# Optimization experiments

Measured on AMD Instinct MI355X. Metric: run time of the kernel, lower is better.

Reference implementation:

```python
import jax, jax.numpy as jnp
import numpy as np

K = 3
KK = K * K
G = 8  # num_heads / offset groups
PAD = K // 2


def conv2d(x, w, b):
    # NCHW conv, stride 1, same padding
    y = jax.lax.conv_general_dilated(
        x, w, window_strides=(1, 1), padding=[(PAD, PAD), (PAD, PAD)],
        dimension_numbers=("NCHW", "OIHW", "NCHW"))
    return y + b[None, :, None, None]


def bilinear_sample(img, py, px):
    # img: [Cg, H, W]; py/px: [KK, H, W] fractional sampling locations
    # zero-padding bilinear (torchvision deform_conv2d semantics)
    Cg, H, W = img.shape
    flat = img.reshape(Cg, H * W)

    y0 = jnp.floor(py)
    x0 = jnp.floor(px)
    wy1 = py - y0
    wx1 = px - x0
    wy0 = 1.0 - wy1
    wx0 = 1.0 - wx1
    y0i = y0.astype(jnp.int32)
    x0i = x0.astype(jnp.int32)

    def gather(iy, ix):
        valid = (iy >= 0) & (iy < H) & (ix >= 0) & (ix < W)
        idx = jnp.clip(iy, 0, H - 1) * W + jnp.clip(ix, 0, W - 1)
        v = jnp.take(flat, idx.reshape(-1), axis=1).reshape(Cg, KK, H, W)
        return v * valid[None].astype(img.dtype)

    return (gather(y0i, x0i) * (wy0 * wx0)[None]
            + gather(y0i, x0i + 1) * (wy0 * wx1)[None]
            + gather(y0i + 1, x0i) * (wy1 * wx0)[None]
            + gather(y0i + 1, x0i + 1) * (wy1 * wx1)[None])


def setup_inputs() -> dict:
    key = jax.random.key(0)
    ks = jax.random.split(key, 8)
    B, C, H, W = 8, 256, 64, 64
    O = 256
    x = jax.random.normal(ks[0], (B, C, H, W), jnp.float32)
    w_off = jax.random.normal(ks[1], (2 * KK * G, C, K, K), jnp.float32) * 0.01
    b_off = jax.random.normal(ks[2], (2 * KK * G,), jnp.float32) * 0.01
    w_attn = jax.random.normal(ks[3], (KK * G, C, K, K), jnp.float32) * 0.01
    b_attn = jax.random.normal(ks[4], (KK * G,), jnp.float32) * 0.01
    w_out = jax.random.normal(ks[5], (O, C, K, K), jnp.float32) * 0.02
    b_out = jax.random.normal(ks[6], (O,), jnp.float32) * 0.01
    return {"x": x, "w_off": w_off, "b_off": b_off,
            "w_attn": w_attn, "b_attn": b_attn,
            "w_out": w_out, "b_out": b_out}


def reference(x, w_off, b_off, w_attn, b_attn, w_out, b_out):
    B, C, H, W = x.shape
    O = w_out.shape[0]
    Cg = C // G

    # learned offsets: [B, G, KK, 2(dy,dx), H, W]
    off = conv2d(x, w_off, b_off).reshape(B, G, KK, 2, H, W)
    # modulation mask with softmax over the KK kernel taps (per head)
    attn = conv2d(x, w_attn, b_attn).reshape(B, G, KK, H, W)
    attn = jax.nn.softmax(attn, axis=2)

    # base sampling grid for each kernel tap (stride=1, dilation=1)
    ki = (jnp.arange(KK) // K).astype(x.dtype)  # kernel row
    kj = (jnp.arange(KK) % K).astype(x.dtype)   # kernel col
    base_y = jnp.arange(H, dtype=x.dtype)[None, :, None] - PAD + ki[:, None, None]  # [KK,H,1]
    base_x = jnp.arange(W, dtype=x.dtype)[None, None, :] - PAD + kj[:, None, None]  # [KK,1,W]
    py = base_y + off[:, :, :, 0]  # [B,G,KK,H,W]
    px = base_x + off[:, :, :, 1]

    xg = x.reshape(B, G, Cg, H, W)
    # vmap bilinear gather over batch and offset groups -> [B,G,Cg,KK,H,W]
    samp = jax.vmap(jax.vmap(bilinear_sample))(xg, py, px)

    # modulated deformable conv: mask-weight the samples, contract with weights
    wt = w_out.reshape(O, G, Cg, KK)
    out = jnp.einsum("bgnkhw,bgkhw,ognk->bohw", samp, attn, wt)
    return out + b_out[None, :, None, None]
```

## Files before the change

kernel.cpp:

```cpp
#include <hip/hip_runtime.h>

#define BN   8
#define CC   256
#define HH   64
#define WW   64
#define GG   8
#define CG   32
#define KKK  9
#define OO   256
#define HW   (HH*WW)
#define NPAD 256
#define NOUT 216

typedef __attribute__((ext_vector_type(8))) _Float16 half8;
typedef __attribute__((ext_vector_type(4))) float f32x4;

union U4H8 { uint4 u; half8 h; };

#define LGKM0_BARRIER() do { \
    asm volatile("s_waitcnt lgkmcnt(0)" ::: "memory"); \
    __builtin_amdgcn_s_barrier(); \
    __builtin_amdgcn_sched_barrier(0); \
} while (0)

__global__ void repack_w(const float* __restrict__ w_out, _Float16* __restrict__ wt3) {
    int idx = blockIdx.x * 256 + threadIdx.x;
    if (idx >= GG * KKK * CG * OO) return;
    int e    = idx & 7;
    int lane = (idx >> 3) & 63;
    int ot   = (idx >> 9) & 15;
    int s    = idx >> 13;
    int kk = s % 9;
    int g  = s / 9;
    int oc = ot * 16 + (lane & 15);
    int cg = (lane >> 4) * 8 + e;
    wt3[idx] = (_Float16)w_out[oc * 2304 + (g * 32 + cg) * 9 + kk];
}

__global__ void repack_conv(const float* __restrict__ w_off, const float* __restrict__ b_off,
                            const float* __restrict__ w_attn, const float* __restrict__ b_attn,
                            _Float16* __restrict__ wt_conv, float* __restrict__ bias_c) {
    int idx = blockIdx.x * 256 + threadIdx.x;
    if (idx >= 9 * NPAD * 256) return;
    int e    = idx & 7;
    int lane = (idx >> 3) & 63;
    int ot   = (idx >> 9) & 15;
    int gs   = idx >> 13;
    int tap = gs >> 3;
    int ch  = (gs & 7) * 32 + (lane >> 4) * 8 + e;
    int n   = ot * 16 + (lane & 15);
    float v = 0.f;
    if (n < 144)      v = w_off[(n * 256 + ch) * 9 + tap];
    else if (n < 216) v = w_attn[((n - 144) * 256 + ch) * 9 + tap];
    wt_conv[idx] = (_Float16)v;
    if (idx < 224) {
        float bv = 0.f;
        if (idx < 144)      bv = b_off[idx];
        else if (idx < 216) bv = b_attn[idx - 144];
        bias_c[idx] = bv;
    }
}

__global__ __launch_bounds__(256) void repack_x(const float* __restrict__ x,
                                                _Float16* __restrict__ x_h) {
    __shared__ _Float16 T[64][264];
    const int bid = blockIdx.x;
    const int b = bid & 7, h = bid >> 3;
    const int t = threadIdx.x;
    const float* src = x + (((long)(b * 256 + t)) << 12) + h * 64;
    #pragma unroll
    for (int i = 0; i < 16; ++i) {
        float4 f = ((const float4*)src)[i];
        T[i * 4 + 0][t] = (_Float16)f.x;
        T[i * 4 + 1][t] = (_Float16)f.y;
        T[i * 4 + 2][t] = (_Float16)f.z;
        T[i * 4 + 3][t] = (_Float16)f.w;
    }
    __syncthreads();
    _Float16* dst = x_h + (((long)(b * 4096 + h * 64)) << 8);
    #pragma unroll
    for (int it = 0; it < 8; ++it) {
        int idx = it * 256 + t;
        int px = idx >> 5, ch = idx & 31;
        uint4 v = *(const uint4*)&T[px][ch * 8];
        *(uint4*)(dst + px * 256 + ch * 8) = v;
    }
}

__global__ __launch_bounds__(512, 4) void conv_mfma(
    const _Float16* __restrict__ x_h, const _Float16* __restrict__ wt_conv,
    const float* __restrict__ bias_c, float* __restrict__ conv_buf) {
    __shared__ alignas(16) char smem[36864];
    _Float16 (*Ald)[2][64][40] = (_Float16 (*)[2][64][40])smem;
    float* red = (float*)smem;

    const int bid = blockIdx.x;
    const int b = bid & 7, h = bid >> 3;
    const int t = threadIdx.x;
    const int lane = t & 63;
    const int wv = t >> 6;
    const int group = wv >> 2;
    const int wg = wv & 3;
    const int tl = t & 255;
    const int px = tl >> 2, cq = tl & 3;
    const int gs0 = group * 36;

    f32x4 acc[4][4];
    #pragma unroll
    for (int i = 0; i < 4; ++i)
        #pragma unroll
        for (int j = 0; j < 4; ++j) acc[i][j] = (f32x4){0.f, 0.f, 0.f, 0.f};

    const _Float16* xb = x_h + ((long)b << 20) + cq * 8;
    const _Float16* wB = wt_conv + (long)(wg * 256 + lane) * 8;

    uint4 aR; bool vA;
    uint4 bq0, bq1, bq2, bq3;

    {
        int tap = gs0 >> 3, cc = gs0 & 7;
        int y = h + tap / 3 - 1, xc = px + tap % 3 - 1;
        bool v0 = ((unsigned)y < 64u) && ((unsigned)xc < 64u);
        int yc = min(max(y, 0), 63), xcc = min(max(xc, 0), 63);
        uint4 a0 = *(const uint4*)(xb + ((long)(yc * 64 + xcc)) * 256 + cc * 32);
        uint4 az = v0 ? a0 : make_uint4(0u, 0u, 0u, 0u);
        *(uint4*)&Ald[group][0][px][cq * 8] = az;
    }
    {
        int gsn = gs0 + 1;
        int tap = gsn >> 3, cc = gsn & 7;
        int y = h + tap / 3 - 1, xc = px + tap % 3 - 1;
        vA = ((unsigned)y < 64u) && ((unsigned)xc < 64u);
        int yc = min(max(y, 0), 63), xcc = min(max(xc, 0), 63);
        aR = *(const uint4*)(xb + ((long)(yc * 64 + xcc)) * 256 + cc * 32);
    }
    {
        const _Float16* wsB = wB + (long)gs0 * 8192;
        bq0 = *(const uint4*)(wsB);
        bq1 = *(const uint4*)(wsB + 512);
        bq2 = *(const uint4*)(wsB + 1024);
        bq3 = *(const uint4*)(wsB + 1536);
    }
    LGKM0_BARRIER();

    for (int s = 0; s < 36; ++s) {
        const int gs = gs0 + s;
        if (s < 35) {
            uint4 az = vA ? aR : make_uint4(0u, 0u, 0u, 0u);
            *(uint4*)&Ald[group][(s + 1) & 1][px][cq * 8] = az;
        }
        if (s < 34) {
            int gsn = gs + 2;
            int tap = gsn >> 3, cc = gsn & 7;
            int y = h + tap / 3 - 1, xc = px + tap % 3 - 1;
            vA = ((unsigned)y < 64u) && ((unsigned)xc < 64u);
            int yc = min(max(y, 0), 63), xcc = min(max(xc, 0), 63);
            aR = *(const uint4*)(xb + ((long)(yc * 64 + xcc)) * 256 + cc * 32);
        }
        {
            const int k0 = (lane >> 4) * 8;
            U4H8 b0, b1, b2, b3; b0.u = bq0; b1.u = bq1; b2.u = bq2; b3.u = bq3;
            #pragma unroll
            for (int mi = 0; mi < 4; ++mi) {
                half8 a = *(const half8*)&Ald[group][s & 1][mi * 16 + (lane & 15)][k0];
                acc[mi][0] = __builtin_amdgcn_mfma_f32_16x16x32_f16(a, b0.h, acc[mi][0], 0, 0, 0);
                acc[mi][1] = __builtin_amdgcn_mfma_f32_16x16x32_f16(a, b1.h, acc[mi][1], 0, 0, 0);
                acc[mi][2] = __builtin_amdgcn_mfma_f32_16x16x32_f16(a, b2.h, acc[mi][2], 0, 0, 0);
                acc[mi][3] = __builtin_amdgcn_mfma_f32_16x16x32_f16(a, b3.h, acc[mi][3], 0, 0, 0);
            }
        }
        if (s < 35) {
            const _Float16* wsB = wB + (long)(gs + 1) * 8192;
            bq0 = *(const uint4*)(wsB);
            bq1 = *(const uint4*)(wsB + 512);
            bq2 = *(const uint4*)(wsB + 1024);
            bq3 = *(const uint4*)(wsB + 1536);
        }
        LGKM0_BARRIER();
    }

    #pragma unroll
    for (int r = 0; r < 2; ++r) {
        __syncthreads();
        if (group == 1) {
            #pragma unroll
            for (int m2 = 0; m2 < 2; ++m2)
                #pragma unroll
                for (int j = 0; j < 4; ++j)
                    *(f32x4*)&red[tl * 36 + m2 * 16 + j * 4] = acc[r * 2 + m2][j];
        }
        __syncthreads();
        if (group == 0) {
            #pragma unroll
            for (int m2 = 0; m2 < 2; ++m2)
                #pragma unroll
                for (int j = 0; j < 4; ++j) {
                    f32x4 v = *(const f32x4*)&red[tl * 36 + m2 * 16 + j * 4];
                    acc[r * 2 + m2][j] += v;
                }
        }
    }

    if (group == 0) {
        const int colb = (lane >> 4) * 4;
        #pragma unroll
        for (int mi = 0; mi < 4; ++mi) {
            int px0 = mi * 16 + colb;
            #pragma unroll
            for (int j = 0; j < 4; ++j) {
                int oc = wg * 64 + j * 16 + (lane & 15);
                if (oc < NOUT) {
                    float bb = bias_c[oc];
                    float4 v = make_float4(acc[mi][j][0] + bb, acc[mi][j][1] + bb,
                                           acc[mi][j][2] + bb, acc[mi][j][3] + bb);
                    *(float4*)&conv_buf[((long)b * NOUT + oc) * HW + h * WW + px0] = v;
                }
            }
        }
    }
}

__device__ __forceinline__ void calc_coords(int h, int px, int ki, int kj,
    float dy, float dx,
    int& i00, int& i01, int& i10, int& i11,
    float& u00, float& u01, float& u10, float& u11) {
    float py  = (float)(h - 1 + ki) + dy;
    float pxf = (float)(px - 1 + kj) + dx;
    float y0f = floorf(py), x0f = floorf(pxf);
    int y0 = (int)y0f, x0 = (int)x0f;
    float wy1 = py - y0f, wx1 = pxf - x0f;
    float wy0 = 1.f - wy1, wx0 = 1.f - wx1;
    int y1 = y0 + 1, x1 = x0 + 1;
    float m00 = (((unsigned)y0 < 64u) && ((unsigned)x0 < 64u)) ? 1.f : 0.f;
    float m01 = (((unsigned)y0 < 64u) && ((unsigned)x1 < 64u)) ? 1.f : 0.f;
    float m10 = (((unsigned)y1 < 64u) && ((unsigned)x0 < 64u)) ? 1.f : 0.f;
    float m11 = (((unsigned)y1 < 64u) && ((unsigned)x1 < 64u)) ? 1.f : 0.f;
    int cy0 = min(max(y0, 0), 63), cy1 = min(max(y1, 0), 63);
    int cx0 = min(max(x0, 0), 63), cx1 = min(max(x1, 0), 63);
    u00 = wy0 * wx0 * m00; u01 = wy0 * wx1 * m01;
    u10 = wy1 * wx0 * m10; u11 = wy1 * wx1 * m11;
    i00 = cy0 * 64 + cx0; i01 = cy0 * 64 + cx1;
    i10 = cy1 * 64 + cx0; i11 = cy1 * 64 + cx1;
}

__global__ __launch_bounds__(512, 4) void sample_gemm_mfma(
    const _Float16* __restrict__ x_h, const float* __restrict__ conv_buf,
    const _Float16* __restrict__ wt3,
    const float* __restrict__ b_out, float* __restrict__ out) {
    __shared__ alignas(16) char smem[38912];
    _Float16 (*Ald)[2][64][40] = (_Float16 (*)[2][64][40])smem;
    float* attnL = (float*)(smem + 20480);
    float* red = (float*)smem;

    const int bid = blockIdx.x;
    const int b = bid & 7, h = bid >> 3;
    const int t = threadIdx.x;
    const int lane = t & 63;
    const int wv = t >> 6;
    const int group = wv >> 2;
    const int wg = wv & 3;
    const int tl = t & 255;
    const int px = tl >> 2, cq = tl & 3;
    const int gs0 = group * 36;

    f32x4 acc[4][4];
    #pragma unroll
    for (int i = 0; i < 4; ++i)
        #pragma unroll
        for (int j = 0; j < 4; ++j) acc[i][j] = (f32x4){0.f, 0.f, 0.f, 0.f};

    const float* cbase = conv_buf + (long)b * NOUT * HW + h * WW;
    const _Float16* xbase = x_h + ((long)b << 20) + cq * 8;
    const _Float16* wB3 = wt3 + (long)(wg * 256 + lane) * 8;

    {
        int ppx = t & 63, g = t >> 6;
        const float* ap = cbase + (long)(144 + g * 9) * HW + ppx;
        float v[9];
        float m = -1e30f;
        #pragma unroll
        for (int k = 0; k < 9; ++k) { v[k] = ap[k * HW]; m = fmaxf(m, v[k]); }
        float ssum = 0.f;
        #pragma unroll
        for (int k = 0; k < 9; ++k) { v[k] = __expf(v[k] - m); ssum += v[k]; }
        float inv = 1.f / ssum;
        #pragma unroll
        for (int k = 0; k < 9; ++k) attnL[(g * 9 + k) * 64 + ppx] = v[k] * inv;
    }
    float dy0 = cbase[(2 * gs0) * HW + px], dx0 = cbase[(2 * gs0 + 1) * HW + px];
    __syncthreads();

    uint4 q00, q01, q10, q11;
    float u00, u01, u10, u11;
    float dyN, dxN;
    uint4 bq0, bq1, bq2, bq3;
    {
        int i00, i01, i10, i11;
        float v00, v01, v10, v11;
        calc_coords(h, px, 0, 0, dy0, dx0, i00, i01, i10, i11, v00, v01, v10, v11);
        const _Float16* xg = xbase + (group * 4) * 32;
        uint4 a00 = *(const uint4*)(xg + (long)i00 * 256);
        uint4 a01 = *(const uint4*)(xg + (long)i01 * 256);
        uint4 a10 = *(const uint4*)(xg + (long)i10 * 256);
        uint4 a11 = *(const uint4*)(xg + (long)i11 * 256);
        float av = attnL[gs0 * 64 + px];
        U4H8 h00, h01, h10, h11;
        h00.u = a00; h01.u = a01; h10.u = a10; h11.u = a11;
        half8 rr = h00.h * (_Float16)v00 + h01.h * (_Float16)v01
                 + h10.h * (_Float16)v10 + h11.h * (_Float16)v11;
        rr = rr * (_Float16)av;
        *(half8*)&Ald[group][0][px][cq * 8] = rr;
    }
    {
        float dy1 = cbase[(2 * (gs0 + 1)) * HW + px];
        float dx1 = cbase[(2 * (gs0 + 1) + 1) * HW + px];
        int i00, i01, i10, i11;
        calc_coords(h, px, 0, 1, dy1, dx1, i00, i01, i10, i11, u00, u01, u10, u11);
        const _Float16* xg = xbase + (group * 4) * 32;
        q00 = *(const uint4*)(xg + (long)i00 * 256);
        q01 = *(const uint4*)(xg + (long)i01 * 256);
        q10 = *(const uint4*)(xg + (long)i10 * 256);
        q11 = *(const uint4*)(xg + (long)i11 * 256);
        dyN = cbase[(2 * (gs0 + 2)) * HW + px];
        dxN = cbase[(2 * (gs0 + 2) + 1) * HW + px];
    }
    {
        const _Float16* wsB = wB3 + (long)gs0 * 8192;
        bq0 = *(const uint4*)(wsB);
        bq1 = *(const uint4*)(wsB + 512);
        bq2 = *(const uint4*)(wsB + 1024);
        bq3 = *(const uint4*)(wsB + 1536);
    }
    LGKM0_BARRIER();

    for (int s = 0; s < 36; ++s) {
        const int gs = gs0 + s;
        if (s < 35) {
            float av = attnL[(gs + 1) * 64 + px];
            U4H8 a00, a01, a10, a11;
            a00.u = q00; a01.u = q01; a10.u = q10; a11.u = q11;
            half8 rr = a00.h * (_Float16)u00 + a01.h * (_Float16)u01
                     + a10.h * (_Float16)u10 + a11.h * (_Float16)u11;
            rr = rr * (_Float16)av;
            *(half8*)&Ald[group][(s + 1) & 1][px][cq * 8] = rr;
        }
        if (s < 34) {
            int sn = s + 2;
            int g = group * 4 + sn / 9, kk = sn % 9;
            int i00, i01, i10, i11;
            calc_coords(h, px, kk / 3, kk % 3, dyN, dxN, i00, i01, i10, i11,
                        u00, u01, u10, u11);
            const _Float16* xg = xbase + g * 32;
            q00 = *(const uint4*)(xg + (long)i00 * 256);
            q01 = *(const uint4*)(xg + (long)i01 * 256);
            q10 = *(const uint4*)(xg + (long)i10 * 256);
            q11 = *(const uint4*)(xg + (long)i11 * 256);
            int s3 = min(s + 3, 35);
            dyN = cbase[(2 * (gs0 + s3)) * HW + px];
            dxN = cbase[(2 * (gs0 + s3) + 1) * HW + px];
        }
        {
            const int k0 = (lane >> 4) * 8;
            U4H8 b0, b1, b2, b3; b0.u = bq0; b1.u = bq1; b2.u = bq2; b3.u = bq3;
            #pragma unroll
            for (int mi = 0; mi < 4; ++mi) {
                half8 a = *(const half8*)&Ald[group][s & 1][mi * 16 + (lane & 15)][k0];
                acc[mi][0] = __builtin_amdgcn_mfma_f32_16x16x32_f16(a, b0.h, acc[mi][0], 0, 0, 0);
                acc[mi][1] = __builtin_amdgcn_mfma_f32_16x16x32_f16(a, b1.h, acc[mi][1], 0, 0, 0);
                acc[mi][2] = __builtin_amdgcn_mfma_f32_16x16x32_f16(a, b2.h, acc[mi][2], 0, 0, 0);
                acc[mi][3] = __builtin_amdgcn_mfma_f32_16x16x32_f16(a, b3.h, acc[mi][3], 0, 0, 0);
            }
        }
        if (s < 35) {
            const _Float16* wsB = wB3 + (long)(gs + 1) * 8192;
            bq0 = *(const uint4*)(wsB);
            bq1 = *(const uint4*)(wsB + 512);
            bq2 = *(const uint4*)(wsB + 1024);
            bq3 = *(const uint4*)(wsB + 1536);
        }
        LGKM0_BARRIER();
    }

    #pragma unroll
    for (int r = 0; r < 2; ++r) {
        __syncthreads();
        if (group == 1) {
            #pragma unroll
            for (int m2 = 0; m2 < 2; ++m2)
                #pragma unroll
                for (int j = 0; j < 4; ++j)
                    *(f32x4*)&red[tl * 36 + m2 * 16 + j * 4] = acc[r * 2 + m2][j];
        }
        __syncthreads();
        if (group == 0) {
            #pragma unroll
            for (int m2 = 0; m2 < 2; ++m2)
                #pragma unroll
                for (int j = 0; j < 4; ++j) {
                    f32x4 v = *(const f32x4*)&red[tl * 36 + m2 * 16 + j * 4];
                    acc[r * 2 + m2][j] += v;
                }
        }
    }

    if (group == 0) {
        const int colb = (lane >> 4) * 4;
        #pragma unroll
        for (int mi = 0; mi < 4; ++mi) {
            int px0 = mi * 16 + colb;
            #pragma unroll
            for (int j = 0; j < 4; ++j) {
                int oc = wg * 64 + j * 16 + (lane & 15);
                float bb = b_out[oc];
                float4 v = make_float4(acc[mi][j][0] + bb, acc[mi][j][1] + bb,
                                       acc[mi][j][2] + bb, acc[mi][j][3] + bb);
                *(float4*)&out[((long)b * OO + oc) * HW + h * WW + px0] = v;
            }
        }
    }
}

extern "C" void kernel_launch(void* const* d_in, const int* in_sizes, int n_in,
                              void* d_out, int out_size, void* d_ws, size_t ws_size,
                              hipStream_t stream) {
    const float* x      = (const float*)d_in[0];
    const float* w_off  = (const float*)d_in[1];
    const float* b_off  = (const float*)d_in[2];
    const float* w_attn = (const float*)d_in[3];
    const float* b_attn = (const float*)d_in[4];
    const float* w_out  = (const float*)d_in[5];
    const float* b_out  = (const float*)d_in[6];
    float* out = (float*)d_out;

    _Float16* x_h     = (_Float16*)d_ws;
    float* conv_buf   = (float*)(x_h + 8388608);
    _Float16* wt3     = (_Float16*)(conv_buf + 7077888);
    _Float16* wt_conv = wt3 + 589824;
    float* bias_c     = (float*)(wt_conv + 589824);

    repack_w<<<dim3((589824 + 255) / 256), dim3(256), 0, stream>>>(w_out, wt3);
    repack_conv<<<dim3((9 * NPAD * 256 + 255) / 256), dim3(256), 0, stream>>>(
        w_off, b_off, w_attn, b_attn, wt_conv, bias_c);
    repack_x<<<dim3(512), dim3(256), 0, stream>>>(x, x_h);

    conv_mfma<<<dim3(512), dim3(512), 0, stream>>>(x_h, wt_conv, bias_c, conv_buf);

    sample_gemm_mfma<<<dim3(512), dim3(512), 0, stream>>>(
        x_h, conv_buf, wt3, b_out, out);
}
```

Measured before the change: 214.0 us.

## Load conv A-fragments directly from global into registers, dropping LDS staging

The offset/attention conv GEMM kernel no longer stages the im2col A tile through shared memory with per-step barriers. Each wave loads its own MFMA A fragments straight from global memory into registers, with a two-deep register double buffer for A and B. This removes the LDS writes and reads and the barrier every K-step. In exchange, each wave issues redundant global loads of the A tile (four waves per group load the same data), register pressure rises, and launch bounds drop from 4 to 2 blocks per CU.

```diff
diff --git a/kernel.cpp b/kernel.cpp
--- a/kernel.cpp
+++ b/kernel.cpp
@@ -87,12 +87,84 @@
     }
 }
 
-__global__ __launch_bounds__(512, 4) void conv_mfma(
+__device__ __forceinline__ void load_A(const _Float16* xb, int h, int pxl, int gss,
+                                       uint4& A0, uint4& A1, uint4& A2, uint4& A3) {
+    int tap = gss >> 3, cc = gss & 7;
+    int ti = tap / 3, tj = tap % 3;
+    int y = h + ti - 1;
+    bool vy = ((unsigned)y < 64u);
+    int yc = min(max(y, 0), 63);
+    const _Float16* xrow = xb + ((long)(yc * 64)) * 256 + cc * 32;
+    uint4 z = make_uint4(0u, 0u, 0u, 0u);
+    int xc0 = pxl + tj - 1;
+    {
+        int xc = xc0;
+        bool v = vy && ((unsigned)xc < 64u);
+        int xcc = min(max(xc, 0), 63);
+        uint4 a = *(const uint4*)(xrow + (long)xcc * 256);
+        A0 = v ? a : z;
+    }
+    {
+        int xc = xc0 + 16;
+        bool v = vy && ((unsigned)xc < 64u);
+        int xcc = min(max(xc, 0), 63);
+        uint4 a = *(const uint4*)(xrow + (long)xcc * 256);
+        A1 = v ? a : z;
+    }
+    {
+        int xc = xc0 + 32;
+        bool v = vy && ((unsigned)xc < 64u);
+        int xcc = min(max(xc, 0), 63);
+        uint4 a = *(const uint4*)(xrow + (long)xcc * 256);
+        A2 = v ? a : z;
+    }
+    {
+        int xc = xc0 + 48;
+        bool v = vy && ((unsigned)xc < 64u);
+        int xcc = min(max(xc, 0), 63);
+        uint4 a = *(const uint4*)(xrow + (long)xcc * 256);
+        A3 = v ? a : z;
+    }
+}
+
+__device__ __forceinline__ void load_B(const _Float16* wB, int gss,
+                                       uint4& B0, uint4& B1, uint4& B2, uint4& B3) {
+    const _Float16* wsB = wB + (long)gss * 8192;
+    B0 = *(const uint4*)(wsB);
+    B1 = *(const uint4*)(wsB + 512);
+    B2 = *(const uint4*)(wsB + 1024);
+    B3 = *(const uint4*)(wsB + 1536);
+}
+
+__device__ __forceinline__ void mfma_stage(
+    const uint4& A0, const uint4& A1, const uint4& A2, const uint4& A3,
+    const uint4& B0, const uint4& B1, const uint4& B2, const uint4& B3,
+    f32x4 (&acc)[4][4]) {
+    U4H8 a0, a1, a2, a3, b0, b1, b2, b3;
+    a0.u = A0; a1.u = A1; a2.u = A2; a3.u = A3;
+    b0.u = B0; b1.u = B1; b2.u = B2; b3.u = B3;
+    acc[0][0] = __builtin_amdgcn_mfma_f32_16x16x32_f16(a0.h, b0.h, acc[0][0], 0, 0, 0);
+    acc[0][1] = __builtin_amdgcn_mfma_f32_16x16x32_f16(a0.h, b1.h, acc[0][1], 0, 0, 0);
+    acc[0][2] = __builtin_amdgcn_mfma_f32_16x16x32_f16(a0.h, b2.h, acc[0][2], 0, 0, 0);
+    acc[0][3] = __builtin_amdgcn_mfma_f32_16x16x32_f16(a0.h, b3.h, acc[0][3], 0, 0, 0);
+    acc[1][0] = __builtin_amdgcn_mfma_f32_16x16x32_f16(a1.h, b0.h, acc[1][0], 0, 0, 0);
+    acc[1][1] = __builtin_amdgcn_mfma_f32_16x16x32_f16(a1.h, b1.h, acc[1][1], 0, 0, 0);
+    acc[1][2] = __builtin_amdgcn_mfma_f32_16x16x32_f16(a1.h, b2.h, acc[1][2], 0, 0, 0);
+    acc[1][3] = __builtin_amdgcn_mfma_f32_16x16x32_f16(a1.h, b3.h, acc[1][3], 0, 0, 0);
+    acc[2][0] = __builtin_amdgcn_mfma_f32_16x16x32_f16(a2.h, b0.h, acc[2][0], 0, 0, 0);
+    acc[2][1] = __builtin_amdgcn_mfma_f32_16x16x32_f16(a2.h, b1.h, acc[2][1], 0, 0, 0);
+    acc[2][2] = __builtin_amdgcn_mfma_f32_16x16x32_f16(a2.h, b2.h, acc[2][2], 0, 0, 0);
+    acc[2][3] = __builtin_amdgcn_mfma_f32_16x16x32_f16(a2.h, b3.h, acc[2][3], 0, 0, 0);
+    acc[3][0] = __builtin_amdgcn_mfma_f32_16x16x32_f16(a3.h, b0.h, acc[3][0], 0, 0, 0);
+    acc[3][1] = __builtin_amdgcn_mfma_f32_16x16x32_f16(a3.h, b1.h, acc[3][1], 0, 0, 0);
+    acc[3][2] = __builtin_amdgcn_mfma_f32_16x16x32_f16(a3.h, b2.h, acc[3][2], 0, 0, 0);
+    acc[3][3] = __builtin_amdgcn_mfma_f32_16x16x32_f16(a3.h, b3.h, acc[3][3], 0, 0, 0);
+}
+
+__global__ __launch_bounds__(512, 2) void conv_mfma(
     const _Float16* __restrict__ x_h, const _Float16* __restrict__ wt_conv,
     const float* __restrict__ bias_c, float* __restrict__ conv_buf) {
-    __shared__ alignas(16) char smem[36864];
-    _Float16 (*Ald)[2][64][40] = (_Float16 (*)[2][64][40])smem;
-    float* red = (float*)smem;
+    __shared__ alignas(16) float red[9216];
 
     const int bid = blockIdx.x;
     const int b = bid & 7, h = bid >> 3;
@@ -102,8 +174,8 @@
     const int group = wv >> 2;
     const int wg = wv & 3;
     const int tl = t & 255;
-    const int px = tl >> 2, cq = tl & 3;
     const int gs0 = group * 36;
+    const int pxl = lane & 15;
 
     f32x4 acc[4][4];
     #pragma unroll
@@ -111,72 +183,24 @@
         #pragma unroll
         for (int j = 0; j < 4; ++j) acc[i][j] = (f32x4){0.f, 0.f, 0.f, 0.f};
 
-    const _Float16* xb = x_h + ((long)b << 20) + cq * 8;
+    const _Float16* xb = x_h + ((long)b << 20) + (lane >> 4) * 8;
     const _Float16* wB = wt_conv + (long)(wg * 256 + lane) * 8;
 
-    uint4 aR; bool vA;
-    uint4 bq0, bq1, bq2, bq3;
-
-    {
-        int tap = gs0 >> 3, cc = gs0 & 7;
-        int y = h + tap / 3 - 1, xc = px + tap % 3 - 1;
-        bool v0 = ((unsigned)y < 64u) && ((unsigned)xc < 64u);
-        int yc = min(max(y, 0), 63), xcc = min(max(xc, 0), 63);
-        uint4 a0 = *(const uint4*)(xb + ((long)(yc * 64 + xcc)) * 256 + cc * 32);
-        uint4 az = v0 ? a0 : make_uint4(0u, 0u, 0u, 0u);
-        *(uint4*)&Ald[group][0][px][cq * 8] = az;
-    }
-    {
-        int gsn = gs0 + 1;
-        int tap = gsn >> 3, cc = gsn & 7;
-        int y = h + tap / 3 - 1, xc = px + tap % 3 - 1;
-        vA = ((unsigned)y < 64u) && ((unsigned)xc < 64u);
-        int yc = min(max(y, 0), 63), xcc = min(max(xc, 0), 63);
-        aR = *(const uint4*)(xb + ((long)(yc * 64 + xcc)) * 256 + cc * 32);
-    }
-    {
-        const _Float16* wsB = wB + (long)gs0 * 8192;
-        bq0 = *(const uint4*)(wsB);
-        bq1 = *(const uint4*)(wsB + 512);
-        bq2 = *(const uint4*)(wsB + 1024);
-        bq3 = *(const uint4*)(wsB + 1536);
-    }
-    LGKM0_BARRIER();
-
-    for (int s = 0; s < 36; ++s) {
-        const int gs = gs0 + s;
-        if (s < 35) {
-            uint4 az = vA ? aR : make_uint4(0u, 0u, 0u, 0u);
-            *(uint4*)&Ald[group][(s + 1) & 1][px][cq * 8] = az;
-        }
+    uint4 xA0, xA1, xA2, xA3, xB0, xB1, xB2, xB3;
+    uint4 yA0, yA1, yA2, yA3, yB0, yB1, yB2, yB3;
+
+    load_A(xb, h, pxl, gs0, xA0, xA1, xA2, xA3);
+    load_B(wB, gs0, xB0, xB1, xB2, xB3);
+
+    for (int s = 0; s < 36; s += 2) {
+        load_A(xb, h, pxl, gs0 + s + 1, yA0, yA1, yA2, yA3);
+        load_B(wB, gs0 + s + 1, yB0, yB1, yB2, yB3);
+        mfma_stage(xA0, xA1, xA2, xA3, xB0, xB1, xB2, xB3, acc);
         if (s < 34) {
-            int gsn = gs + 2;
-            int tap = gsn >> 3, cc = gsn & 7;
-            int y = h + tap / 3 - 1, xc = px + tap % 3 - 1;
-            vA = ((unsigned)y < 64u) && ((unsigned)xc < 64u);
-            int yc = min(max(y, 0), 63), xcc = min(max(xc, 0), 63);
-            aR = *(const uint4*)(xb + ((long)(yc * 64 + xcc)) * 256 + cc * 32);
-        }
-        {
-            const int k0 = (lane >> 4) * 8;
-            U4H8 b0, b1, b2, b3; b0.u = bq0; b1.u = bq1; b2.u = bq2; b3.u = bq3;
-            #pragma unroll
-            for (int mi = 0; mi < 4; ++mi) {
-                half8 a = *(const half8*)&Ald[group][s & 1][mi * 16 + (lane & 15)][k0];
-                acc[mi][0] = __builtin_amdgcn_mfma_f32_16x16x32_f16(a, b0.h, acc[mi][0], 0, 0, 0);
-                acc[mi][1] = __builtin_amdgcn_mfma_f32_16x16x32_f16(a, b1.h, acc[mi][1], 0, 0, 0);
-                acc[mi][2] = __builtin_amdgcn_mfma_f32_16x16x32_f16(a, b2.h, acc[mi][2], 0, 0, 0);
-                acc[mi][3] = __builtin_amdgcn_mfma_f32_16x16x32_f16(a, b3.h, acc[mi][3], 0, 0, 0);
-            }
-        }
-        if (s < 35) {
-            const _Float16* wsB = wB + (long)(gs + 1) * 8192;
-            bq0 = *(const uint4*)(wsB);
-            bq1 = *(const uint4*)(wsB + 512);
-            bq2 = *(const uint4*)(wsB + 1024);
-            bq3 = *(const uint4*)(wsB + 1536);
-        }
-        LGKM0_BARRIER();
+            load_A(xb, h, pxl, gs0 + s + 2, xA0, xA1, xA2, xA3);
+            load_B(wB, gs0 + s + 2, xB0, xB1, xB2, xB3);
+        }
+        mfma_stage(yA0, yA1, yA2, yA3, yB0, yB1, yB2, yB3, acc);
     }
 
     #pragma unroll
```

New measurement: 255.2 us. 1.19x slower.

## Zero-pad the fp16 activation layout to drop bounds checks in conv and sampling

Applied to the files above, without the earlier changes.

The fp16 NHWC copy of x is stored with a 2-pixel zero border (68x68 spatial), and the buffer is cleared with a memset on every call. The conv kernel then loads its im2col tiles without validity masks or clamping. The bilinear sampler computes a single clamped base index and reaches the four corners by fixed +1 pixel and +1 row offsets, so the four per-corner masks and clamps go away. The goal is less integer and select work in the gather-heavy loops, at the cost of a full-buffer memset per call and a slightly larger workspace.

```diff
diff --git a/kernel.cpp b/kernel.cpp
--- a/kernel.cpp
+++ b/kernel.cpp
@@ -11,6 +11,10 @@
 #define HW   (HH*WW)
 #define NPAD 256
 #define NOUT 216
+
+#define XH   68
+#define XROW (XH*256)
+#define XB   (XH*XH*256)
 
 typedef __attribute__((ext_vector_type(8))) _Float16 half8;
 typedef __attribute__((ext_vector_type(4))) float f32x4;
@@ -77,7 +81,7 @@
         T[i * 4 + 3][t] = (_Float16)f.w;
     }
     __syncthreads();
-    _Float16* dst = x_h + (((long)(b * 4096 + h * 64)) << 8);
+    _Float16* dst = x_h + ((long)(b * XH + h + 2) * XH + 2) * 256;
     #pragma unroll
     for (int it = 0; it < 8; ++it) {
         int idx = it * 256 + t;
@@ -111,28 +115,23 @@
         #pragma unroll
         for (int j = 0; j < 4; ++j) acc[i][j] = (f32x4){0.f, 0.f, 0.f, 0.f};
 
-    const _Float16* xb = x_h + ((long)b << 20) + cq * 8;
+    const _Float16* xb = x_h + (long)b * XB + cq * 8;
     const _Float16* wB = wt_conv + (long)(wg * 256 + lane) * 8;
 
-    uint4 aR; bool vA;
+    uint4 aR;
     uint4 bq0, bq1, bq2, bq3;
 
     {
         int tap = gs0 >> 3, cc = gs0 & 7;
-        int y = h + tap / 3 - 1, xc = px + tap % 3 - 1;
-        bool v0 = ((unsigned)y < 64u) && ((unsigned)xc < 64u);
-        int yc = min(max(y, 0), 63), xcc = min(max(xc, 0), 63);
-        uint4 a0 = *(const uint4*)(xb + ((long)(yc * 64 + xcc)) * 256 + cc * 32);
-        uint4 az = v0 ? a0 : make_uint4(0u, 0u, 0u, 0u);
-        *(uint4*)&Ald[group][0][px][cq * 8] = az;
+        int y = h + tap / 3 + 1, xc = px + tap % 3 + 1;
+        uint4 a0 = *(const uint4*)(xb + ((long)(y * XH + xc)) * 256 + cc * 32);
+        *(uint4*)&Ald[group][0][px][cq * 8] = a0;
     }
     {
         int gsn = gs0 + 1;
         int tap = gsn >> 3, cc = gsn & 7;
-        int y = h + tap / 3 - 1, xc = px + tap % 3 - 1;
-        vA = ((unsigned)y < 64u) && ((unsigned)xc < 64u);
-        int yc = min(max(y, 0), 63), xcc = min(max(xc, 0), 63);
-        aR = *(const uint4*)(xb + ((long)(yc * 64 + xcc)) * 256 + cc * 32);
+        int y = h + tap / 3 + 1, xc = px + tap % 3 + 1;
+        aR = *(const uint4*)(xb + ((long)(y * XH + xc)) * 256 + cc * 32);
     }
     {
         const _Float16* wsB = wB + (long)gs0 * 8192;
@@ -146,16 +145,13 @@
     for (int s = 0; s < 36; ++s) {
         const int gs = gs0 + s;
         if (s < 35) {
-            uint4 az = vA ? aR : make_uint4(0u, 0u, 0u, 0u);
-            *(uint4*)&Ald[group][(s + 1) & 1][px][cq * 8] = az;
+            *(uint4*)&Ald[group][(s + 1) & 1][px][cq * 8] = aR;
         }
         if (s < 34) {
             int gsn = gs + 2;
             int tap = gsn >> 3, cc = gsn & 7;
-            int y = h + tap / 3 - 1, xc = px + tap % 3 - 1;
-            vA = ((unsigned)y < 64u) && ((unsigned)xc < 64u);
-            int yc = min(max(y, 0), 63), xcc = min(max(xc, 0), 63);
-            aR = *(const uint4*)(xb + ((long)(yc * 64 + xcc)) * 256 + cc * 32);
+            int y = h + tap / 3 + 1, xc = px + tap % 3 + 1;
+            aR = *(const uint4*)(xb + ((long)(y * XH + xc)) * 256 + cc * 32);
         }
         {
             const int k0 = (lane >> 4) * 8;
@@ -221,26 +217,18 @@
 }
 
 __device__ __forceinline__ void calc_coords(int h, int px, int ki, int kj,
-    float dy, float dx,
-    int& i00, int& i01, int& i10, int& i11,
+    float dy, float dx, int& i00,
     float& u00, float& u01, float& u10, float& u11) {
     float py  = (float)(h - 1 + ki) + dy;
     float pxf = (float)(px - 1 + kj) + dx;
     float y0f = floorf(py), x0f = floorf(pxf);
-    int y0 = (int)y0f, x0 = (int)x0f;
     float wy1 = py - y0f, wx1 = pxf - x0f;
     float wy0 = 1.f - wy1, wx0 = 1.f - wx1;
-    int y1 = y0 + 1, x1 = x0 + 1;
-    float m00 = (((unsigned)y0 < 64u) && ((unsigned)x0 < 64u)) ? 1.f : 0.f;
-    float m01 = (((unsigned)y0 < 64u) && ((unsigned)x1 < 64u)) ? 1.f : 0.f;
-    float m10 = (((unsigned)y1 < 64u) && ((unsigned)x0 < 64u)) ? 1.f : 0.f;
-    float m11 = (((unsigned)y1 < 64u) && ((unsigned)x1 < 64u)) ? 1.f : 0.f;
-    int cy0 = min(max(y0, 0), 63), cy1 = min(max(y1, 0), 63);
-    int cx0 = min(max(x0, 0), 63), cx1 = min(max(x1, 0), 63);
-    u00 = wy0 * wx0 * m00; u01 = wy0 * wx1 * m01;
-    u10 = wy1 * wx0 * m10; u11 = wy1 * wx1 * m11;
-    i00 = cy0 * 64 + cx0; i01 = cy0 * 64 + cx1;
-    i10 = cy1 * 64 + cx0; i11 = cy1 * 64 + cx1;
+    int y0 = min(max((int)y0f, -2), 64);
+    int x0 = min(max((int)x0f, -2), 64);
+    u00 = wy0 * wx0; u01 = wy0 * wx1;
+    u10 = wy1 * wx0; u11 = wy1 * wx1;
+    i00 = (y0 + 2) * XH + (x0 + 2);
 }
 
 __global__ __launch_bounds__(512, 4) void sample_gemm_mfma(
@@ -270,7 +258,7 @@
         for (int j = 0; j < 4; ++j) acc[i][j] = (f32x4){0.f, 0.f, 0.f, 0.f};
 
     const float* cbase = conv_buf + (long)b * NOUT * HW + h * WW;
-    const _Float16* xbase = x_h + ((long)b << 20) + cq * 8;
+    const _Float16* xbase = x_h + (long)b * XB + cq * 8;
     const _Float16* wB3 = wt3 + (long)(wg * 256 + lane) * 8;
 
     {
@@ -295,14 +283,14 @@
     float dyN, dxN;
     uint4 bq0, bq1, bq2, bq3;
     {
-        int i00, i01, i10, i11;
+        int i00;
         float v00, v01, v10, v11;
-        calc_coords(h, px, 0, 0, dy0, dx0, i00, i01, i10, i11, v00, v01, v10, v11);
-        const _Float16* xg = xbase + (group * 4) * 32;
-        uint4 a00 = *(const uint4*)(xg + (long)i00 * 256);
-        uint4 a01 = *(const uint4*)(xg + (long)i01 * 256);
-        uint4 a10 = *(const uint4*)(xg + (long)i10 * 256);
-        uint4 a11 = *(const uint4*)(xg + (long)i11 * 256);
+        calc_coords(h, px, 0, 0, dy0, dx0, i00, v00, v01, v10, v11);
+        const _Float16* xg = xbase + (group * 4) * 32 + (long)i00 * 256;
+        uint4 a00 = *(const uint4*)(xg);
+        uint4 a01 = *(const uint4*)(xg + 256);
+        uint4 a10 = *(const uint4*)(xg + XROW);
+        uint4 a11 = *(const uint4*)(xg + XROW + 256);
         float av = attnL[gs0 * 64 + px];
         U4H8 h00, h01, h10, h11;
         h00.u = a00; h01.u = a01; h10.u = a10; h11.u = a11;
@@ -314,13 +302,13 @@
     {
         float dy1 = cbase[(2 * (gs0 + 1)) * HW + px];
         float dx1 = cbase[(2 * (gs0 + 1) + 1) * HW + px];
-        int i00, i01, i10, i11;
-        calc_coords(h, px, 0, 1, dy1, dx1, i00, i01, i10, i11, u00, u01, u10, u11);
-        const _Float16* xg = xbase + (group * 4) * 32;
-        q00 = *(const uint4*)(xg + (long)i00 * 256);
-        q01 = *(const uint4*)(xg + (long)i01 * 256);
-        q10 = *(const uint4*)(xg + (long)i10 * 256);
-        q11 = *(const uint4*)(xg + (long)i11 * 256);
+        int i00;
+        calc_coords(h, px, 0, 1, dy1, dx1, i00, u00, u01, u10, u11);
+        const _Float16* xg = xbase + (group * 4) * 32 + (long)i00 * 256;
+        q00 = *(const uint4*)(xg);
+        q01 = *(const uint4*)(xg + 256);
+        q10 = *(const uint4*)(xg + XROW);
+        q11 = *(const uint4*)(xg + XROW + 256);
         dyN = cbase[(2 * (gs0 + 2)) * HW + px];
         dxN = cbase[(2 * (gs0 + 2) + 1) * HW + px];
     }
@@ -347,14 +335,13 @@
         if (s < 34) {
             int sn = s + 2;
             int g = group * 4 + sn / 9, kk = sn % 9;
-            int i00, i01, i10, i11;
-            calc_coords(h, px, kk / 3, kk % 3, dyN, dxN, i00, i01, i10, i11,
-                        u00, u01, u10, u11);
-            const _Float16* xg = xbase + g * 32;
-            q00 = *(const uint4*)(xg + (long)i00 * 256);
-            q01 = *(const uint4*)(xg + (long)i01 * 256);
-            q10 = *(const uint4*)(xg + (long)i10 * 256);
-            q11 = *(const uint4*)(xg + (long)i11 * 256);
+            int i00;
+            calc_coords(h, px, kk / 3, kk % 3, dyN, dxN, i00, u00, u01, u10, u11);
+            const _Float16* xg = xbase + g * 32 + (long)i00 * 256;
+            q00 = *(const uint4*)(xg);
+            q01 = *(const uint4*)(xg + 256);
+            q10 = *(const uint4*)(xg + XROW);
+            q11 = *(const uint4*)(xg + XROW + 256);
             int s3 = min(s + 3, 35);
             dyN = cbase[(2 * (gs0 + s3)) * HW + px];
             dxN = cbase[(2 * (gs0 + s3) + 1) * HW + px];
@@ -433,10 +420,12 @@
     float* out = (float*)d_out;
 
     _Float16* x_h     = (_Float16*)d_ws;
-    float* conv_buf   = (float*)(x_h + 8388608);
+    float* conv_buf   = (float*)(x_h + 9469952);
     _Float16* wt3     = (_Float16*)(conv_buf + 7077888);
     _Float16* wt_conv = wt3 + 589824;
     float* bias_c     = (float*)(wt_conv + 589824);
+
+    hipMemsetAsync(x_h, 0, (size_t)9469952 * sizeof(_Float16), stream);
 
     repack_w<<<dim3((589824 + 255) / 256), dim3(256), 0, stream>>>(w_out, wt3);
     repack_conv<<<dim3((9 * NPAD * 256 + 255) / 256), dim3(256), 0, stream>>>(
```

After: 215.9 us. Within noise of the previous version (+0.9%).
